# Kernel optimization log

Hardware: AMD Instinct MI355X
Metric: run time of the kernel (lower is better)

## Reference

```python
import jax, jax.numpy as jnp
import numpy as np

R_MIN = 0.01
R_MAX = 0.6
H = 32            # polar radial bins (after pooling)
W = 64            # polar angular bins (after pooling)
UP_R = 10         # radial upsampling factor
UP_T = 10         # angular upsampling factor
ATT_ALPHA = 5.0
B, C, IMG = 64, 3, 224


def _conv(x, w, b):
    # NCHW valid conv, stride 1 (matches nn.Conv2d default padding=0)
    y = jax.lax.conv_general_dilated(x, w, (1, 1), 'VALID',
                                     dimension_numbers=('NCHW', 'OIHW', 'NCHW'))
    return y + b[None, :, None, None]


def _maxpool2(x):
    return jax.lax.reduce_window(x, -jnp.inf, jax.lax.max,
                                 (1, 1, 2, 2), (1, 1, 2, 2), 'VALID')


def _grid_sample_border(x, grid):
    # F.grid_sample, bilinear, padding_mode='border', align_corners=False
    Bn, Cn, Hi, Wi = x.shape
    ix = ((grid[..., 0] + 1.0) * Wi - 1.0) * 0.5   # x-coord -> width index
    iy = ((grid[..., 1] + 1.0) * Hi - 1.0) * 0.5   # y-coord -> height index
    x0f = jnp.floor(ix)
    y0f = jnp.floor(iy)
    wx = (ix - x0f)[..., None]
    wy = (iy - y0f)[..., None]
    x0 = jnp.clip(x0f.astype(jnp.int32), 0, Wi - 1)
    x1 = jnp.clip(x0f.astype(jnp.int32) + 1, 0, Wi - 1)
    y0 = jnp.clip(y0f.astype(jnp.int32), 0, Hi - 1)
    y1 = jnp.clip(y0f.astype(jnp.int32) + 1, 0, Hi - 1)
    bidx = jnp.arange(Bn)[:, None, None]
    v00 = x[bidx, :, y0, x0]   # [B,Hg,Wg,C]
    v01 = x[bidx, :, y0, x1]
    v10 = x[bidx, :, y1, x0]
    v11 = x[bidx, :, y1, x1]
    out = (v00 * (1 - wx) * (1 - wy) + v01 * wx * (1 - wy)
           + v10 * (1 - wx) * wy + v11 * wx * wy)
    return jnp.transpose(out, (0, 3, 1, 2))  # [B,C,Hg,Wg]


def setup_inputs() -> dict:
    key = jax.random.key(0)
    ks = jax.random.split(key, 10)
    x = jax.random.normal(ks[0], (B, C, IMG, IMG), dtype=jnp.float32)
    l_t_prev = jax.random.uniform(ks[1], (B, 2), dtype=jnp.float32)
    conv1_w = jax.random.normal(ks[2], (6, C, 5, 5), dtype=jnp.float32) * 0.1
    conv1_b = jnp.zeros((6,), jnp.float32)
    conv2_w = jax.random.normal(ks[3], (16, 6, 5, 5), dtype=jnp.float32) * 0.1
    conv2_b = jnp.zeros((16,), jnp.float32)
    fc1_w = jax.random.normal(ks[4], (8, 16), dtype=jnp.float32) * 0.1
    fc1_b = jnp.zeros((8,), jnp.float32)
    fc2_w = jax.random.normal(ks[5], (2, 8), dtype=jnp.float32) * 0.1
    fc2_b = jnp.zeros((2,), jnp.float32)
    return dict(x=x, l_t_prev=l_t_prev, conv1_w=conv1_w, conv1_b=conv1_b,
                conv2_w=conv2_w, conv2_b=conv2_b, fc1_w=fc1_w, fc1_b=fc1_b,
                fc2_w=fc2_w, fc2_b=fc2_b)


def reference(x, l_t_prev, conv1_w, conv1_b, conv2_w, conv2_b,
              fc1_w, fc1_b, fc2_w, fc2_b):
    # --- attention branch: conv -> maxpool -> conv -> GAP -> fc -> sigmoid ---
    h = _conv(x, conv1_w, conv1_b)
    h = _maxpool2(h)
    h = _conv(h, conv2_w, conv2_b)
    feat = h.mean(axis=(2, 3))                     # AdaptiveAvgPool2d(1), [B,16]
    h = jax.nn.relu(feat @ fc1_w.T + fc1_b)
    weight = jax.nn.sigmoid(h @ fc2_w.T + fc2_b) * ATT_ALPHA   # [B,2]
    # --- per-batch log-polar grid ---
    Hg, Wg = H * UP_R, W * UP_T
    angle = 2.0 * jnp.pi * jnp.arange(Wg, dtype=jnp.float32) / Wg
    unit = jnp.stack([jnp.sin(angle), jnp.cos(angle)], axis=-1)   # [Wg,2]
    start = jnp.log(R_MIN * weight[:, 0])
    stop = jnp.log(R_MAX * weight[:, 1])
    t = jnp.arange(Hg, dtype=jnp.float32) / (Hg - 1)
    radii = jnp.exp(start[:, None] + (stop - start)[:, None] * t[None])  # [B,Hg]
    grid = radii[:, :, None, None] * unit[None, None]     # [B,Hg,Wg,2]
    grid = grid + l_t_prev[:, None, None, :]
    # --- irregular bilinear sampling + box filter ---
    sampled = _grid_sample_border(x, grid)                 # [B,C,Hg,Wg]
    Bn, Cn = sampled.shape[:2]
    pooled = sampled.reshape(Bn, Cn, H, UP_R, W, UP_T).mean(axis=(3, 5))
    return pooled, weight
```

## Files before the change

### kernel.cpp

```cpp
#include <hip/hip_runtime.h>
#include <math.h>

#define Bn    64
#define Cn    3
#define IMG   224
#define PLANE (IMG*IMG)
#define C1    6
#define P1    110
#define P2    106
#define NVALID (P2*P2)
#define Hh    32
#define Ww    64
#define UPR   10
#define UPT   10
#define Hg    (Hh*UPR)
#define Wg    (Ww*UPT)
#define POOLED_SIZE (Bn*Cn*Hh*Ww)
#define NCHUNK 28
#define PSTRIDE 152
#define ROWB  (IMG*8)
#define TPB1  448

typedef unsigned short u16;
typedef unsigned long long ull;
typedef _Float16 h8v __attribute__((ext_vector_type(8)));
typedef float f4v __attribute__((ext_vector_type(4)));

#define PART_FLOATS ((size_t)Bn * NCHUNK * PSTRIDE)
#define X4B_U16     ((size_t)Bn * PLANE * 4)
#define WS_NEEDED   ((PART_FLOATS + Bn * 2) * 4 + X4B_U16 * 2)

__device__ __forceinline__ unsigned hpack(float a, float b) {
    union { _Float16 h; u16 u; } x, y;
    x.h = (_Float16)a; y.h = (_Float16)b;
    return (unsigned)x.u | ((unsigned)y.u << 16);
}
__device__ __forceinline__ float h2lo(unsigned v) {
    union { _Float16 h; u16 u; } c; c.u = (u16)(v & 0xffffu); return (float)c.h;
}
__device__ __forceinline__ float h2hi(unsigned v) {
    union { _Float16 h; u16 u; } c; c.u = (u16)(v >> 16); return (float)c.h;
}

#define GSHFL(v, idx) __shfl((v), (lane & 48) + (idx), 64)

__global__ __launch_bounds__(TPB1) void k1_fused(
    const float* __restrict__ x,
    const float* __restrict__ w1,
    const float* __restrict__ b1,
    float* __restrict__ partial,
    u16* __restrict__ x4h,
    int do_pack)
{
    __shared__ __attribute__((aligned(16))) unsigned char xs[12 * ROWB + 128];
    __shared__ __attribute__((aligned(16))) _Float16 sa[5][64][8];
    __shared__ float rowR[7][C1][4];
    __shared__ float edgeLo[4][C1][4];
    __shared__ float edgeHi[4][C1][4];

    const int b     = blockIdx.y;
    const int chunk = blockIdx.x;
    const int tid   = threadIdx.x;
    const int wid   = tid >> 6;
    const int lane  = tid & 63;
    const int n     = lane & 15;
    const int g     = lane >> 4;
    const int gy0   = chunk * 8;

    const float* xb = x + (size_t)b * (Cn * PLANE);
    u16* ob = x4h + (size_t)b * PLANE * 4;

    if (wid == 0) {
        #pragma unroll
        for (int ky = 0; ky < 5; ++ky) {
            #pragma unroll
            for (int j = 0; j < 8; ++j) {
                const int kmem = g * 8 + j;
                const int ic = kmem & 3, kx = kmem >> 2;
                float w = 0.0f;
                if (n < C1 && ic < 3 && kx < 5)
                    w = w1[((n * 3 + ic) * 5 + ky) * 5 + kx];
                sa[ky][lane][j] = (_Float16)w;
            }
        }
    } else {
        for (int i = tid - 64; i < 12 * 112; i += TPB1 - 64) {
            const int r = i / 112;
            const int p = i - r * 112;
            const int gy = gy0 + r;
            uint4 U; U.x = U.y = U.z = U.w = 0u;
            if (gy < IMG) {
                const float2 v0 = *(const float2*)(xb + 0 * PLANE + gy * IMG + 2 * p);
                const float2 v1 = *(const float2*)(xb + 1 * PLANE + gy * IMG + 2 * p);
                const float2 v2 = *(const float2*)(xb + 2 * PLANE + gy * IMG + 2 * p);
                U.x = hpack(v0.x, v1.x);
                U.y = hpack(v2.x, 0.0f);
                U.z = hpack(v0.y, v1.y);
                U.w = hpack(v2.y, 0.0f);
            }
            *(uint4*)(xs + r * ROWB + p * 16) = U;
            if (do_pack && r < 8)
                *(uint4*)(ob + ((size_t)gy * IMG + 2 * p) * 4) = U;
        }
    }
    __syncthreads();

    h8v a[5];
    #pragma unroll
    for (int ky = 0; ky < 5; ++ky) a[ky] = *(const h8v*)&sa[ky][lane][0];
    f4v binit;
    #pragma unroll
    for (int e = 0; e < 4; ++e) {
        const int oc = g * 4 + e;
        binit[e] = (oc < C1) ? b1[oc] : 0.0f;
    }

    float colsum[4][4];
    #pragma unroll
    for (int py = 0; py < 4; ++py)
        #pragma unroll
        for (int e = 0; e < 4; ++e) colsum[py][e] = 0.0f;

    #pragma unroll
    for (int si = 0; si < 2; ++si) {
        const int s = wid * 2 + si;
        const unsigned sByte = (unsigned)(s * 128 + n * 8 + g * 16);

        f4v acc[8];
        #pragma unroll
        for (int q = 0; q < 8; ++q) acc[q] = binit;

        #pragma unroll
        for (int r = 0; r < 12; ++r) {
            h8v bf;
            const unsigned char* bp = xs + r * ROWB + sByte;
            ((ull*)&bf)[0] = *(const ull*)bp;
            ((ull*)&bf)[1] = *(const ull*)(bp + 8);
            #pragma unroll
            for (int ky = 0; ky < 5; ++ky) {
                const int q = r - ky;
                if (q >= 0 && q < 8)
                    acc[q] = __builtin_amdgcn_mfma_f32_16x16x32_f16(
                        a[ky], bf, acc[q], 0, 0, 0);
            }
        }

        #pragma unroll
        for (int py = 0; py < 4; ++py) {
            #pragma unroll
            for (int e = 0; e < 4; ++e) {
                float t = fmaxf(acc[2 * py][e], acc[2 * py + 1][e]);
                t = fmaxf(t, __shfl_xor(t, 1, 64));
                if (s == 13 && n >= 12) t = 0.0f;
                colsum[py][e] += t;
                const int oc = g * 4 + e;
                if (s == 0) {
                    const float c0 = GSHFL(t, 0), c1 = GSHFL(t, 2);
                    const float c2 = GSHFL(t, 4), c3 = GSHFL(t, 6);
                    const float S1 = c0, S2 = S1 + c1, S3 = S2 + c2, S4 = S3 + c3;
                    const float sv = (n == 0) ? S1 : (n == 1) ? S2 : (n == 2) ? S3 : S4;
                    if (n < 4 && oc < C1) edgeLo[py][oc][n] = sv;
                }
                if (s == 13) {
                    const float d109 = GSHFL(t, 10), d108 = GSHFL(t, 8);
                    const float d107 = GSHFL(t, 6),  d106 = GSHFL(t, 4);
                    const float U1 = d109, U2 = U1 + d108, U3 = U2 + d107, U4 = U3 + d106;
                    const float uv = (n == 0) ? U1 : (n == 1) ? U2 : (n == 2) ? U3 : U4;
                    if (n < 4 && oc < C1) edgeHi[py][oc][n] = uv;
                }
            }
        }
    }

    #pragma unroll
    for (int py = 0; py < 4; ++py) {
        #pragma unroll
        for (int e = 0; e < 4; ++e) {
            float v = colsum[py][e];
            v += __shfl_xor(v, 2, 64);
            v += __shfl_xor(v, 4, 64);
            v += __shfl_xor(v, 8, 64);
            const int oc = g * 4 + e;
            if (n == 0 && oc < C1) rowR[wid][oc][py] = v;
        }
    }
    __syncthreads();

    if (tid < 150) {
        const int oc = tid / 25;
        const int rem = tid - oc * 25;
        const int ky = rem / 5, kx = rem - ky * 5;
        float total = 0.0f;
        #pragma unroll
        for (int py = 0; py < 4; ++py) {
            const int y = chunk * 4 + py;
            const bool valid = (y < P1) && ((unsigned)(y - ky) <= 105u);
            float v = rowR[0][oc][py] + rowR[1][oc][py] + rowR[2][oc][py]
                    + rowR[3][oc][py] + rowR[4][oc][py] + rowR[5][oc][py]
                    + rowR[6][oc][py];
            if (kx > 0) v -= edgeLo[py][oc][kx - 1];
            if (kx < 4) v -= edgeHi[py][oc][3 - kx];
            total += valid ? v : 0.0f;
        }
        partial[((size_t)b * NCHUNK + chunk) * PSTRIDE + tid] = total;
    }
}

#define K3_HEAD_BODY                                                          \
    if (tid < 150) {                                                          \
        const float* p = partial + (size_t)b * NCHUNK * PSTRIDE + tid;        \
        float s = 0.0f;                                                       \
        _Pragma("unroll")                                                     \
        for (int c = 0; c < NCHUNK; ++c) s += p[c * PSTRIDE];                 \
        wsb[tid] = s;                                                         \
    }                                                                         \
    __syncthreads();                                                          \
    if (tid < 16) {                                                           \
        float s = 0.0f;                                                       \
        for (int j = 0; j < 150; ++j) s += w2[tid * 150 + j] * wsb[j];        \
        sfeat[tid] = b2[tid] + s * (1.0f / (float)NVALID);                    \
    }                                                                         \
    __syncthreads();                                                          \
    if (tid < 8) {                                                            \
        float s = fc1b[tid];                                                  \
        _Pragma("unroll")                                                     \
        for (int j = 0; j < 16; ++j) s += fc1w[tid * 16 + j] * sfeat[j];      \
        sh[tid] = fmaxf(s, 0.0f);                                             \
    }                                                                         \
    __syncthreads();                                                          \
    if (tid < 2) {                                                            \
        float s = fc2b[tid];                                                  \
        _Pragma("unroll")                                                     \
        for (int j = 0; j < 8; ++j) s += fc2w[tid * 8 + j] * sh[j];           \
        float sig = (s >= 0.0f) ? (1.0f / (1.0f + expf(-s)))                  \
                                : (expf(s) / (1.0f + expf(s)));               \
        const float wgt = 5.0f * sig;                                         \
        sWt[tid] = wgt;                                                       \
        out[POOLED_SIZE + b * 2 + tid] = wgt;                                 \
    }                                                                         \
    __syncthreads();

__device__ __forceinline__ void sample_coords(
    float gxn, float gyn, int& x0, int& y0, float& wx, float& wy)
{
    float ix = ((gxn + 1.0f) * (float)IMG - 1.0f) * 0.5f;
    float iy = ((gyn + 1.0f) * (float)IMG - 1.0f) * 0.5f;
    ix = fminf(fmaxf(ix, 0.0f), (float)(IMG - 1));
    iy = fminf(fmaxf(iy, 0.0f), (float)(IMG - 1));
    x0 = (int)ix; if (x0 > IMG - 2) x0 = IMG - 2;
    y0 = (int)iy; if (y0 > IMG - 2) y0 = IMG - 2;
    wx = ix - (float)x0;
    wy = iy - (float)y0;
}

__global__ __launch_bounds__(640) void k3_sample_pool_f16(
    const u16* __restrict__ x4h,
    const float* __restrict__ ltp,
    const float* __restrict__ partial,
    const float* __restrict__ w2,  const float* __restrict__ b2,
    const float* __restrict__ fc1w, const float* __restrict__ fc1b,
    const float* __restrict__ fc2w, const float* __restrict__ fc2b,
    float* __restrict__ out)
{
    __shared__ float part[3 * Wg];
    __shared__ float wsb[150];
    __shared__ float sfeat[16];
    __shared__ float sh[8];
    __shared__ float sWt[2];

    const int L = blockIdx.x;
    const int q = L >> 3;
    const int h = q & 31;
    const int b = (L & 7) + 8 * (q >> 5);
    const int tid = threadIdx.x;

    K3_HEAD_BODY

    const float w0 = sWt[0];
    const float w1 = sWt[1];
    const float l0 = ltp[b * 2 + 0];
    const float l1 = ltp[b * 2 + 1];
    const float start = logf(0.01f * w0);
    const float stop  = logf(0.6f  * w1);
    const float dr = stop - start;

    const float angle = 6.283185307179586f * (float)tid / (float)Wg;
    const float sn = __sinf(angle);
    const float cs = __cosf(angle);

    const u16* xb4 = x4h + (size_t)b * PLANE * 4;

    const float ratio = expf(dr * (1.0f / (float)(Hg - 1)));
    float r = expf(start + dr * ((float)(h * UPR) / (float)(Hg - 1)));

    float acc0 = 0.0f, acc1 = 0.0f, acc2 = 0.0f;
    #pragma unroll
    for (int i = 0; i < UPR; ++i) {
        int x0, y0; float wx, wy;
        sample_coords(r * sn + l0, r * cs + l1, x0, y0, wx, wy);
        r *= ratio;

        const u16* base = xb4 + ((size_t)(y0 * IMG + x0)) * 4;
        const uint4 R0 = *(const uint4*)(base);
        const uint4 R1 = *(const uint4*)(base + IMG * 4);

        const float wx0 = 1.0f - wx, wy0 = 1.0f - wy;
        const float w00 = wx0 * wy0, w01 = wx * wy0;
        const float w10 = wx0 * wy,  w11 = wx * wy;

        acc0 += w00*h2lo(R0.x) + w01*h2lo(R0.z) + w10*h2lo(R1.x) + w11*h2lo(R1.z);
        acc1 += w00*h2hi(R0.x) + w01*h2hi(R0.z) + w10*h2hi(R1.x) + w11*h2hi(R1.z);
        acc2 += w00*h2lo(R0.y) + w01*h2lo(R0.w) + w10*h2lo(R1.y) + w11*h2lo(R1.w);
    }
    part[0 * Wg + tid] = acc0;
    part[1 * Wg + tid] = acc1;
    part[2 * Wg + tid] = acc2;
    __syncthreads();

    if (tid < Cn * Ww) {
        const int c = tid / Ww;
        const int w = tid % Ww;
        const float* p = part + c * Wg + w * UPT;
        float s = 0.0f;
        #pragma unroll
        for (int j = 0; j < UPT; ++j) s += p[j];
        out[(((size_t)b * Cn + c) * Hh + h) * Ww + w] = s * (1.0f / (UPR * UPT));
    }
}

__global__ __launch_bounds__(640) void k3_sample_pool_nchw(
    const float* __restrict__ x, const float* __restrict__ ltp,
    const float* __restrict__ partial,
    const float* __restrict__ w2,  const float* __restrict__ b2,
    const float* __restrict__ fc1w, const float* __restrict__ fc1b,
    const float* __restrict__ fc2w, const float* __restrict__ fc2b,
    float* __restrict__ out)
{
    __shared__ float part[3 * Wg];
    __shared__ float wsb[150];
    __shared__ float sfeat[16];
    __shared__ float sh[8];
    __shared__ float sWt[2];

    const int L = blockIdx.x;
    const int q = L >> 3;
    const int h = q & 31;
    const int b = (L & 7) + 8 * (q >> 5);
    const int tid = threadIdx.x;

    K3_HEAD_BODY

    const float w0 = sWt[0];
    const float w1 = sWt[1];
    const float l0 = ltp[b * 2 + 0];
    const float l1 = ltp[b * 2 + 1];
    const float start = logf(0.01f * w0);
    const float stop  = logf(0.6f  * w1);
    const float dr = stop - start;
    const float angle = 6.283185307179586f * (float)tid / (float)Wg;
    const float sn = __sinf(angle);
    const float cs = __cosf(angle);
    const float* xb = x + (size_t)b * Cn * PLANE;

    const float ratio = expf(dr * (1.0f / (float)(Hg - 1)));
    float r = expf(start + dr * ((float)(h * UPR) / (float)(Hg - 1)));

    float acc0 = 0.0f, acc1 = 0.0f, acc2 = 0.0f;
    #pragma unroll
    for (int i = 0; i < UPR; ++i) {
        int x0, y0; float wx, wy;
        sample_coords(r * sn + l0, r * cs + l1, x0, y0, wx, wy);
        r *= ratio;
        const float wx0 = 1.0f - wx, wy0 = 1.0f - wy;
        const float w00 = wx0 * wy0, w01 = wx * wy0;
        const float w10 = wx0 * wy,  w11 = wx * wy;
        const int o00 = y0 * IMG + x0;
        acc0 += w00*xb[o00] + w01*xb[o00+1] + w10*xb[o00+IMG] + w11*xb[o00+IMG+1];
        const float* x1p = xb + PLANE;
        acc1 += w00*x1p[o00] + w01*x1p[o00+1] + w10*x1p[o00+IMG] + w11*x1p[o00+IMG+1];
        const float* x2p = xb + 2 * PLANE;
        acc2 += w00*x2p[o00] + w01*x2p[o00+1] + w10*x2p[o00+IMG] + w11*x2p[o00+IMG+1];
    }
    part[0 * Wg + tid] = acc0;
    part[1 * Wg + tid] = acc1;
    part[2 * Wg + tid] = acc2;
    __syncthreads();

    if (tid < Cn * Ww) {
        const int c = tid / Ww;
        const int w = tid % Ww;
        const float* p = part + c * Wg + w * UPT;
        float s = 0.0f;
        #pragma unroll
        for (int j = 0; j < UPT; ++j) s += p[j];
        out[(((size_t)b * Cn + c) * Hh + h) * Ww + w] = s * (1.0f / (UPR * UPT));
    }
}

extern "C" void kernel_launch(void* const* d_in, const int* in_sizes, int n_in,
                              void* d_out, int out_size, void* d_ws, size_t ws_size,
                              hipStream_t stream) {
    const float* x       = (const float*)d_in[0];
    const float* ltp     = (const float*)d_in[1];
    const float* conv1_w = (const float*)d_in[2];
    const float* conv1_b = (const float*)d_in[3];
    const float* conv2_w = (const float*)d_in[4];
    const float* conv2_b = (const float*)d_in[5];
    const float* fc1_w   = (const float*)d_in[6];
    const float* fc1_b   = (const float*)d_in[7];
    const float* fc2_w   = (const float*)d_in[8];
    const float* fc2_b   = (const float*)d_in[9];
    float* out = (float*)d_out;

    const int do_pack = (ws_size >= WS_NEEDED) ? 1 : 0;

    float* part_ws = (float*)d_ws;
    u16*   x4h     = (u16*)(part_ws + PART_FLOATS + Bn * 2);

    k1_fused<<<dim3(NCHUNK, Bn), dim3(TPB1), 0, stream>>>(
        x, conv1_w, conv1_b, part_ws, x4h, do_pack);
    if (do_pack)
        k3_sample_pool_f16<<<dim3(Hh * Bn), dim3(Wg), 0, stream>>>(
            x4h, ltp, part_ws, conv2_w, conv2_b,
            fc1_w, fc1_b, fc2_w, fc2_b, out);
    else
        k3_sample_pool_nchw<<<dim3(Hh * Bn), dim3(Wg), 0, stream>>>(
            x, ltp, part_ws, conv2_w, conv2_b,
            fc1_w, fc1_b, fc2_w, fc2_b, out);
}
```

Measured before the change: 184.9 us.

## Move attention head into last conv block via atomic reduction and completion counter

Conv1 blocks now atomically add their per-chunk partial sums into a per-batch accumulator instead of writing separate partials. The last block to finish, found through a global counter, runs the conv2/GAP/fc/sigmoid head for all batches and writes the attention weights to workspace. The sampling kernel then reads the precomputed weights instead of repeating the head in each of its 2048 blocks. This adds a memset launch, float atomics that make summation order nondeterministic, and a serial tail on a single block.

```diff
diff --git a/kernel.cpp b/kernel.cpp
--- a/kernel.cpp
+++ b/kernel.cpp
@@ -7,8 +7,7 @@
 #define PLANE (IMG*IMG)
 #define C1    6
 #define P1    110
-#define P2    106
-#define NVALID (P2*P2)
+#define NVALID (106*106)
 #define Hh    32
 #define Ww    64
 #define UPR   10
@@ -17,7 +16,8 @@
 #define Wg    (Ww*UPT)
 #define POOLED_SIZE (Bn*Cn*Hh*Ww)
 #define NCHUNK 28
-#define PSTRIDE 152
+#define NBLK1  (NCHUNK*Bn)
+#define WSTRIDE 152
 #define ROWB  (IMG*8)
 #define TPB1  448
 
@@ -26,9 +26,13 @@
 typedef _Float16 h8v __attribute__((ext_vector_type(8)));
 typedef float f4v __attribute__((ext_vector_type(4)));
 
-#define PART_FLOATS ((size_t)Bn * NCHUNK * PSTRIDE)
+#define WSUM_FLOATS (Bn*WSTRIDE)
+#define CTR_OFF     WSUM_FLOATS
+#define WT_OFF      (WSUM_FLOATS + 4)
+#define X4H_OFF_F   9864
 #define X4B_U16     ((size_t)Bn * PLANE * 4)
-#define WS_NEEDED   ((PART_FLOATS + Bn * 2) * 4 + X4B_U16 * 2)
+#define WS_NEEDED   ((size_t)X4H_OFF_F * 4 + X4B_U16 * 2)
+#define MEMSET_BYTES ((CTR_OFF + 1) * 4)
 
 __device__ __forceinline__ unsigned hpack(float a, float b) {
     union { _Float16 h; u16 u; } x, y;
@@ -48,8 +52,15 @@
     const float* __restrict__ x,
     const float* __restrict__ w1,
     const float* __restrict__ b1,
-    float* __restrict__ partial,
+    const float* __restrict__ w2,
+    const float* __restrict__ b2,
+    const float* __restrict__ fc1w, const float* __restrict__ fc1b,
+    const float* __restrict__ fc2w, const float* __restrict__ fc2b,
+    float* __restrict__ wsum,
+    unsigned* __restrict__ counter,
+    float* __restrict__ wt_ws,
     u16* __restrict__ x4h,
+    float* __restrict__ out,
     int do_pack)
 {
     __shared__ __attribute__((aligned(16))) unsigned char xs[12 * ROWB + 128];
@@ -57,9 +68,13 @@
     __shared__ float rowR[7][C1][4];
     __shared__ float edgeLo[4][C1][4];
     __shared__ float edgeHi[4][C1][4];
-
-    const int b     = blockIdx.y;
-    const int chunk = blockIdx.x;
+    __shared__ float sfeat[16][16];
+    __shared__ float shh[16][8];
+    __shared__ unsigned lastFlag;
+
+    const int l     = blockIdx.x;
+    const int b     = l & 63;
+    const int chunk = l >> 6;
     const int tid   = threadIdx.x;
     const int wid   = tid >> 6;
     const int lane  = tid & 63;
@@ -202,43 +217,57 @@
             if (kx < 4) v -= edgeHi[py][oc][3 - kx];
             total += valid ? v : 0.0f;
         }
-        partial[((size_t)b * NCHUNK + chunk) * PSTRIDE + tid] = total;
-    }
-}
-
-#define K3_HEAD_BODY                                                          \
-    if (tid < 150) {                                                          \
-        const float* p = partial + (size_t)b * NCHUNK * PSTRIDE + tid;        \
-        float s = 0.0f;                                                       \
-        _Pragma("unroll")                                                     \
-        for (int c = 0; c < NCHUNK; ++c) s += p[c * PSTRIDE];                 \
-        wsb[tid] = s;                                                         \
-    }                                                                         \
-    __syncthreads();                                                          \
-    if (tid < 16) {                                                           \
-        float s = 0.0f;                                                       \
-        for (int j = 0; j < 150; ++j) s += w2[tid * 150 + j] * wsb[j];        \
-        sfeat[tid] = b2[tid] + s * (1.0f / (float)NVALID);                    \
-    }                                                                         \
-    __syncthreads();                                                          \
-    if (tid < 8) {                                                            \
-        float s = fc1b[tid];                                                  \
-        _Pragma("unroll")                                                     \
-        for (int j = 0; j < 16; ++j) s += fc1w[tid * 16 + j] * sfeat[j];      \
-        sh[tid] = fmaxf(s, 0.0f);                                             \
-    }                                                                         \
-    __syncthreads();                                                          \
-    if (tid < 2) {                                                            \
-        float s = fc2b[tid];                                                  \
-        _Pragma("unroll")                                                     \
-        for (int j = 0; j < 8; ++j) s += fc2w[tid * 8 + j] * sh[j];           \
-        float sig = (s >= 0.0f) ? (1.0f / (1.0f + expf(-s)))                  \
-                                : (expf(s) / (1.0f + expf(s)));               \
-        const float wgt = 5.0f * sig;                                         \
-        sWt[tid] = wgt;                                                       \
-        out[POOLED_SIZE + b * 2 + tid] = wgt;                                 \
-    }                                                                         \
-    __syncthreads();
+        atomicAdd(&wsum[b * WSTRIDE + tid], total);
+    }
+
+    __threadfence();
+    __syncthreads();
+    if (tid == 0) {
+        const unsigned old = atomicAdd(counter, 1u);
+        lastFlag = (old == (unsigned)(NBLK1 - 1)) ? 1u : 0u;
+    }
+    __syncthreads();
+    if (!lastFlag) return;
+
+    float* hw = (float*)xs;
+    for (int batch = 0; batch < 4; ++batch) {
+        const int b0 = batch * 16;
+        for (int i = tid; i < 16 * 150; i += TPB1) {
+            const int bl = i / 150, j = i - bl * 150;
+            hw[bl * WSTRIDE + j] = __hip_atomic_load(
+                &wsum[(b0 + bl) * WSTRIDE + j],
+                __ATOMIC_ACQUIRE, __HIP_MEMORY_SCOPE_AGENT);
+        }
+        __syncthreads();
+        if (tid < 256) {
+            const int bl = tid >> 4, oc = tid & 15;
+            float s = 0.0f;
+            for (int j = 0; j < 150; ++j) s += w2[oc * 150 + j] * hw[bl * WSTRIDE + j];
+            sfeat[bl][oc] = b2[oc] + s * (1.0f / (float)NVALID);
+        }
+        __syncthreads();
+        if (tid < 128) {
+            const int bl = tid >> 3, o = tid & 7;
+            float s = fc1b[o];
+            #pragma unroll
+            for (int j = 0; j < 16; ++j) s += fc1w[o * 16 + j] * sfeat[bl][j];
+            shh[bl][o] = fmaxf(s, 0.0f);
+        }
+        __syncthreads();
+        if (tid < 32) {
+            const int bl = tid >> 1, c = tid & 1;
+            float s = fc2b[c];
+            #pragma unroll
+            for (int j = 0; j < 8; ++j) s += fc2w[c * 8 + j] * shh[bl][j];
+            const float sig = (s >= 0.0f) ? (1.0f / (1.0f + expf(-s)))
+                                          : (expf(s) / (1.0f + expf(s)));
+            const float wgt = 5.0f * sig;
+            wt_ws[(b0 + bl) * 2 + c] = wgt;
+            out[POOLED_SIZE + (b0 + bl) * 2 + c] = wgt;
+        }
+        __syncthreads();
+    }
+}
 
 __device__ __forceinline__ void sample_coords(
     float gxn, float gyn, int& x0, int& y0, float& wx, float& wy)
@@ -256,17 +285,10 @@
 __global__ __launch_bounds__(640) void k3_sample_pool_f16(
     const u16* __restrict__ x4h,
     const float* __restrict__ ltp,
-    const float* __restrict__ partial,
-    const float* __restrict__ w2,  const float* __restrict__ b2,
-    const float* __restrict__ fc1w, const float* __restrict__ fc1b,
-    const float* __restrict__ fc2w, const float* __restrict__ fc2b,
+    const float* __restrict__ wt,
     float* __restrict__ out)
 {
     __shared__ float part[3 * Wg];
-    __shared__ float wsb[150];
-    __shared__ float sfeat[16];
-    __shared__ float sh[8];
-    __shared__ float sWt[2];
 
     const int L = blockIdx.x;
     const int q = L >> 3;
@@ -274,10 +296,8 @@
     const int b = (L & 7) + 8 * (q >> 5);
     const int tid = threadIdx.x;
 
-    K3_HEAD_BODY
-
-    const float w0 = sWt[0];
-    const float w1 = sWt[1];
+    const float w0 = wt[b * 2 + 0];
+    const float w1 = wt[b * 2 + 1];
     const float l0 = ltp[b * 2 + 0];
     const float l1 = ltp[b * 2 + 1];
     const float start = logf(0.01f * w0);
@@ -330,28 +350,17 @@
 
 __global__ __launch_bounds__(640) void k3_sample_pool_nchw(
     const float* __restrict__ x, const float* __restrict__ ltp,
-    const float* __restrict__ partial,
-    const float* __restrict__ w2,  const float* __restrict__ b2,
-    const float* __restrict__ fc1w, const float* __restrict__ fc1b,
-    const float* __restrict__ fc2w, const float* __restrict__ fc2b,
-    float* __restrict__ out)
+    const float* __restrict__ wt, float* __restrict__ out)
 {
     __shared__ float part[3 * Wg];
-    __shared__ float wsb[150];
-    __shared__ float sfeat[16];
-    __shared__ float sh[8];
-    __shared__ float sWt[2];
-
     const int L = blockIdx.x;
     const int q = L >> 3;
     const int h = q & 31;
     const int b = (L & 7) + 8 * (q >> 5);
     const int tid = threadIdx.x;
 
-    K3_HEAD_BODY
-
-    const float w0 = sWt[0];
-    const float w1 = sWt[1];
+    const float w0 = wt[b * 2 + 0];
+    const float w1 = wt[b * 2 + 1];
     const float l0 = ltp[b * 2 + 0];
     const float l1 = ltp[b * 2 + 1];
     const float start = logf(0.01f * w0);
@@ -414,17 +423,20 @@
 
     const int do_pack = (ws_size >= WS_NEEDED) ? 1 : 0;
 
-    float* part_ws = (float*)d_ws;
-    u16*   x4h     = (u16*)(part_ws + PART_FLOATS + Bn * 2);
-
-    k1_fused<<<dim3(NCHUNK, Bn), dim3(TPB1), 0, stream>>>(
-        x, conv1_w, conv1_b, part_ws, x4h, do_pack);
+    float*    wsum    = (float*)d_ws;
+    unsigned* counter = (unsigned*)(wsum + CTR_OFF);
+    float*    wt_ws   = wsum + WT_OFF;
+    u16*      x4h     = (u16*)(wsum + X4H_OFF_F);
+
+    hipMemsetAsync(wsum, 0, MEMSET_BYTES, stream);
+
+    k1_fused<<<dim3(NBLK1), dim3(TPB1), 0, stream>>>(
+        x, conv1_w, conv1_b, conv2_w, conv2_b,
+        fc1_w, fc1_b, fc2_w, fc2_b,
+        wsum, counter, wt_ws, x4h, out, do_pack);
+
     if (do_pack)
-        k3_sample_pool_f16<<<dim3(Hh * Bn), dim3(Wg), 0, stream>>>(
-            x4h, ltp, part_ws, conv2_w, conv2_b,
-            fc1_w, fc1_b, fc2_w, fc2_b, out);
+        k3_sample_pool_f16<<<dim3(Hh * Bn), dim3(Wg), 0, stream>>>(x4h, ltp, wt_ws, out);
     else
-        k3_sample_pool_nchw<<<dim3(Hh * Bn), dim3(Wg), 0, stream>>>(
-            x, ltp, part_ws, conv2_w, conv2_b,
-            fc1_w, fc1_b, fc2_w, fc2_b, out);
-}
+        k3_sample_pool_nchw<<<dim3(Hh * Bn), dim3(Wg), 0, stream>>>(x, ltp, wt_ws, out);
+}
```

After: 375.6 us. 103% more time.
